# Kernel tuning notes

Measured on AMD Instinct MI355X. Metric: run time of the kernel, lower is better.

## Reference

```python
import jax, jax.numpy as jnp
import numpy as np

N_NODES, N_EDGES = 20000, 400000
IN_DIM, HC, OUT_DIM, EDGE_DIM = 128, 128, 128, 2


def _add_self_loops(src, dst, ea, n):
    # PyG fill_value='mean': self-loop edge_attr = mean of incoming edge_attr
    deg = jax.ops.segment_sum(jnp.ones(src.shape[0], ea.dtype), dst, num_segments=n)
    mean_ea = jax.ops.segment_sum(ea, dst, num_segments=n) / jnp.clip(deg, 1.0)[:, None]
    loop = jnp.arange(n, dtype=src.dtype)
    return (jnp.concatenate([src, loop]), jnp.concatenate([dst, loop]),
            jnp.concatenate([ea, mean_ea], axis=0))


def _gat(x, src, dst, ea, W, att_s, att_d, We, att_e, b, heads, out_ch, concat):
    n = x.shape[0]
    xh = (x @ W).reshape(n, heads, out_ch)                      # [N,H,C]
    a_src = jnp.einsum('nhc,hc->nh', xh, att_s)                  # [N,H]
    a_dst = jnp.einsum('nhc,hc->nh', xh, att_d)
    eh = (ea @ We).reshape(-1, heads, out_ch)                    # [E,H,C]
    a_e = jnp.einsum('ehc,hc->eh', eh, att_e)                    # [E,H]
    alpha = jax.nn.leaky_relu(a_src[src] + a_dst[dst] + a_e, 0.2)
    # segment softmax over destination nodes (every node has a self loop)
    amax = jax.ops.segment_max(alpha, dst, num_segments=n)
    amax = jnp.where(jnp.isfinite(amax), amax, 0.0)
    ex = jnp.exp(alpha - amax[dst])
    denom = jax.ops.segment_sum(ex, dst, num_segments=n)
    w = ex / (denom[dst] + 1e-16)                                # [E,H]
    out = jax.ops.segment_sum(xh[src] * w[..., None], dst, num_segments=n)  # [N,H,C]
    out = out.reshape(n, heads * out_ch) if concat else out.mean(axis=1)
    return out + b


def setup_inputs() -> dict:
    key = jax.random.key(0)
    ks = jax.random.split(key, 16)
    g = lambda k, shape, fan: jax.random.normal(k, shape, jnp.float32) * (1.0 / np.sqrt(fan))
    inp = {
        'x': jax.random.normal(ks[0], (N_NODES, IN_DIM), jnp.float32),
        'edge_index': jax.random.randint(ks[1], (2, N_EDGES), 0, N_NODES, jnp.int32),
        'edge_attr': jax.random.normal(ks[2], (N_EDGES, EDGE_DIM), jnp.float32),
        # conv1: GATConv(128 -> hc=128, heads=2, edge_dim=2, concat=True)
        'W1': g(ks[3], (IN_DIM, 2 * HC), IN_DIM),
        'att_s1': g(ks[4], (2, HC), HC),
        'att_d1': g(ks[5], (2, HC), HC),
        'We1': g(ks[6], (EDGE_DIM, 2 * HC), EDGE_DIM),
        'att_e1': g(ks[7], (2, HC), HC),
        'b1': jnp.zeros((2 * HC,), jnp.float32),
        # conv2: GATConv(256 -> 128, heads=1, edge_dim=2, concat=False)
        'W2': g(ks[8], (2 * HC, OUT_DIM), 2 * HC),
        'att_s2': g(ks[9], (1, OUT_DIM), OUT_DIM),
        'att_d2': g(ks[10], (1, OUT_DIM), OUT_DIM),
        'We2': g(ks[11], (EDGE_DIM, OUT_DIM), EDGE_DIM),
        'att_e2': g(ks[12], (1, OUT_DIM), OUT_DIM),
        'b2': jnp.zeros((OUT_DIM,), jnp.float32),
    }
    return inp


def reference(x, edge_index, edge_attr, W1, att_s1, att_d1, We1, att_e1, b1,
              W2, att_s2, att_d2, We2, att_e2, b2):
    n = x.shape[0]
    src0, dst0 = edge_index[0], edge_index[1]
    src, dst, ea = _add_self_loops(src0, dst0, edge_attr, n)
    x0 = x
    h = jax.nn.relu(_gat(x, src, dst, ea, W1, att_s1, att_d1, We1, att_e1, b1,
                         heads=2, out_ch=HC, concat=True))
    h = _gat(h, src, dst, ea, W2, att_s2, att_d2, We2, att_e2, b2,
             heads=1, out_ch=OUT_DIM, concat=False)
    # SimpleConv(aggr='mean'): mean over incoming neighbors on the ORIGINAL edges
    deg = jax.ops.segment_sum(jnp.ones(src0.shape[0], h.dtype), dst0, num_segments=n)
    mean_h = jax.ops.segment_sum(h[src0], dst0, num_segments=n) / jnp.clip(deg, 1.0)[:, None]
    return jax.nn.relu(mean_h + x0)
```

## Files before the change

kernel.cpp:

```cpp
#include <hip/hip_runtime.h>
#include <hip/hip_bf16.h>
#include <hip/hip_fp16.h>

#define NN 20000
#define NE 400000
#define SLOTS 64
#define NBUILD 1563

typedef unsigned short u16;
typedef unsigned int u32;
typedef unsigned long long u64;

typedef __attribute__((ext_vector_type(8))) short bf16x8;
typedef __attribute__((ext_vector_type(4))) float f32x4;

__device__ __forceinline__ float bf2f(u16 u) {
    union { u32 i; float f; } v; v.i = ((u32)u) << 16; return v.f;
}
__device__ __forceinline__ u16 f2bf(float f) {
    __hip_bfloat16 h = __float2bfloat16(f);
    return *reinterpret_cast<u16*>(&h);
}
__device__ __forceinline__ u32 pack2(float lo, float hi) {
    return (u32)f2bf(lo) | ((u32)f2bf(hi) << 16);
}
__device__ __forceinline__ u16 f2h(float f) {
    __half h = __float2half(f);
    return *reinterpret_cast<u16*>(&h);
}
__device__ __forceinline__ float h2f(u16 u) {
    __half h = *reinterpret_cast<__half*>(&u);
    return __half2float(h);
}

__global__ void k_pre(const float* __restrict__ We1, const float* __restrict__ att_e1,
                      const float* __restrict__ We2, const float* __restrict__ att_e2,
                      const float* __restrict__ W1, const float* __restrict__ W2,
                      int* __restrict__ cnt, float* __restrict__ consts,
                      u16* __restrict__ Bt1, u16* __restrict__ Bt2) {
    int idx = blockIdx.x * 256 + threadIdx.x;
    if (idx < NN) cnt[idx] = 0;
    if (idx < 32768) {
        int n = idx >> 7, k = idx & 127;
        Bt1[idx] = f2bf(W1[k * 256 + n]);
    } else {
        int j = idx - 32768;
        int n = j >> 8, k = j & 255;
        Bt2[j] = f2bf(W2[k * 128 + n]);
    }
    if (blockIdx.x == 0) {
        __shared__ float red[128];
        int c = threadIdx.x;
        float p[6];
        if (c < 128) {
            p[0] = We1[0 * 256 + 0 * 128 + c] * att_e1[0 * 128 + c];
            p[1] = We1[0 * 256 + 1 * 128 + c] * att_e1[1 * 128 + c];
            p[2] = We1[1 * 256 + 0 * 128 + c] * att_e1[0 * 128 + c];
            p[3] = We1[1 * 256 + 1 * 128 + c] * att_e1[1 * 128 + c];
            p[4] = We2[0 * 128 + c] * att_e2[c];
            p[5] = We2[1 * 128 + c] * att_e2[c];
        }
        for (int j = 0; j < 6; j++) {
            if (c < 128) red[c] = p[j];
            __syncthreads();
            for (int off = 64; off >= 1; off >>= 1) {
                if (c < off) red[c] += red[c + off];
                __syncthreads();
            }
            if (c == 0) consts[j] = red[0];
            __syncthreads();
        }
    }
}

__global__ __launch_bounds__(256) void k_fat1(const int* __restrict__ ei,
                                              const float* __restrict__ ea,
                                              int* __restrict__ cnt,
                                              uint2* __restrict__ slot,
                                              const float* __restrict__ A,
                                              const u16* __restrict__ Bt,
                                              const float* __restrict__ att_s,
                                              const float* __restrict__ att_d,
                                              u16* __restrict__ C,
                                              float2* __restrict__ a_s,
                                              float2* __restrict__ a_d) {
    if (blockIdx.x < NBUILD) {
        int e = blockIdx.x * 256 + threadIdx.x;
        if (e < NE) {
            int d = ei[NE + e];
            int s = ei[e];
            float2 v = *reinterpret_cast<const float2*>(ea + (size_t)e * 2);
            int pos = atomicAdd(&cnt[d], 1);
            if (pos < SLOTS) {
                u32 eh = (u32)f2h(v.x) | ((u32)f2h(v.y) << 16);
                slot[d * SLOTS + pos] = make_uint2((u32)s, eh);
            }
        }
        return;
    }
    constexpr int K = 128, KC = 4, NT = 16;
    int gb = blockIdx.x - NBUILD;
    int lane = threadIdx.x & 63;
    int wave = threadIdx.x >> 6;
    int r0 = (gb * 4 + wave) * 16;
    if (r0 >= NN) return;
    int mrow = lane & 15, g = lane >> 4;
    int arow = r0 + mrow; if (arow >= NN) arow = NN - 1;
    const float* abase = A + (size_t)arow * K + g * 8;
    bf16x8 a[KC];
#pragma unroll
    for (int kc = 0; kc < KC; kc++) {
        float4 lo = *reinterpret_cast<const float4*>(abase + kc * 32);
        float4 hi = *reinterpret_cast<const float4*>(abase + kc * 32 + 4);
        bf16x8 t;
        t[0] = (short)f2bf(lo.x); t[1] = (short)f2bf(lo.y);
        t[2] = (short)f2bf(lo.z); t[3] = (short)f2bf(lo.w);
        t[4] = (short)f2bf(hi.x); t[5] = (short)f2bf(hi.y);
        t[6] = (short)f2bf(hi.z); t[7] = (short)f2bf(hi.w);
        a[kc] = t;
    }
    f32x4 acc[NT];
#pragma unroll
    for (int nt = 0; nt < NT; nt++) acc[nt] = (f32x4){0.f, 0.f, 0.f, 0.f};
#pragma unroll
    for (int nt = 0; nt < NT; nt++) {
        const u16* bbase = Bt + (size_t)(nt * 16 + mrow) * K + g * 8;
#pragma unroll
        for (int kc = 0; kc < KC; kc++) {
            bf16x8 b = *reinterpret_cast<const bf16x8*>(bbase + kc * 32);
            acc[nt] = __builtin_amdgcn_mfma_f32_16x16x32_bf16(a[kc], b, acc[nt], 0, 0, 0);
        }
    }
    int orow0 = r0 + g * 4;
#pragma unroll
    for (int nt = 0; nt < NT; nt++)
#pragma unroll
        for (int r = 0; r < 4; r++) {
            int rr = orow0 + r;
            if (rr < NN) C[(size_t)rr * 256 + nt * 16 + mrow] = f2bf(acc[nt][r]);
        }
    float attsv[NT], attdv[NT];
#pragma unroll
    for (int nt = 0; nt < NT; nt++) {
        attsv[nt] = att_s[nt * 16 + mrow];
        attdv[nt] = att_d[nt * 16 + mrow];
    }
#pragma unroll
    for (int r = 0; r < 4; r++) {
        float s0 = 0.f, s1 = 0.f, d0 = 0.f, d1 = 0.f;
#pragma unroll
        for (int nt = 0; nt < 8; nt++) { s0 += acc[nt][r] * attsv[nt]; d0 += acc[nt][r] * attdv[nt]; }
#pragma unroll
        for (int nt = 8; nt < NT; nt++) { s1 += acc[nt][r] * attsv[nt]; d1 += acc[nt][r] * attdv[nt]; }
        for (int off = 8; off >= 1; off >>= 1) {
            s0 += __shfl_xor(s0, off); s1 += __shfl_xor(s1, off);
            d0 += __shfl_xor(d0, off); d1 += __shfl_xor(d1, off);
        }
        int rr = orow0 + r;
        if (mrow == 0 && rr < NN) {
            a_s[rr] = make_float2(s0, s1);
            a_d[rr] = make_float2(d0, d1);
        }
    }
}

__global__ __launch_bounds__(256) void k_gemm2(const u16* __restrict__ A,
                                               const u16* __restrict__ Bt,
                                               const float* __restrict__ att_s,
                                               const float* __restrict__ att_d,
                                               u16* __restrict__ C,
                                               float* __restrict__ a_s,
                                               float* __restrict__ a_d) {
    constexpr int K = 256, KC = 8, NT = 8;
    int lane = threadIdx.x & 63;
    int wave = threadIdx.x >> 6;
    int r0 = (blockIdx.x * 4 + wave) * 16;
    if (r0 >= NN) return;
    int mrow = lane & 15, g = lane >> 4;
    int arow = r0 + mrow; if (arow >= NN) arow = NN - 1;
    const u16* abase = A + (size_t)arow * K + g * 8;
    bf16x8 a[KC];
#pragma unroll
    for (int kc = 0; kc < KC; kc++) a[kc] = *reinterpret_cast<const bf16x8*>(abase + kc * 32);
    f32x4 acc[NT];
#pragma unroll
    for (int nt = 0; nt < NT; nt++) acc[nt] = (f32x4){0.f, 0.f, 0.f, 0.f};
#pragma unroll
    for (int nt = 0; nt < NT; nt++) {
        const u16* bbase = Bt + (size_t)(nt * 16 + mrow) * K + g * 8;
#pragma unroll
        for (int kc = 0; kc < KC; kc++) {
            bf16x8 b = *reinterpret_cast<const bf16x8*>(bbase + kc * 32);
            acc[nt] = __builtin_amdgcn_mfma_f32_16x16x32_bf16(a[kc], b, acc[nt], 0, 0, 0);
        }
    }
    int orow0 = r0 + g * 4;
#pragma unroll
    for (int nt = 0; nt < NT; nt++)
#pragma unroll
        for (int r = 0; r < 4; r++) {
            int rr = orow0 + r;
            if (rr < NN) C[(size_t)rr * 128 + nt * 16 + mrow] = f2bf(acc[nt][r]);
        }
    float attsv[NT], attdv[NT];
#pragma unroll
    for (int nt = 0; nt < NT; nt++) {
        attsv[nt] = att_s[nt * 16 + mrow];
        attdv[nt] = att_d[nt * 16 + mrow];
    }
#pragma unroll
    for (int r = 0; r < 4; r++) {
        float s0 = 0.f, d0 = 0.f;
#pragma unroll
        for (int nt = 0; nt < NT; nt++) { s0 += acc[nt][r] * attsv[nt]; d0 += acc[nt][r] * attdv[nt]; }
        for (int off = 8; off >= 1; off >>= 1) {
            s0 += __shfl_xor(s0, off);
            d0 += __shfl_xor(d0, off);
        }
        int rr = orow0 + r;
        if (mrow == 0 && rr < NN) { a_s[rr] = s0; a_d[rr] = d0; }
    }
}

__global__ __launch_bounds__(256) void k_conv1(const int* __restrict__ cnt,
                                               const uint2* __restrict__ slot,
                                               const float* __restrict__ consts,
                                               const u16* __restrict__ xh1,
                                               const float2* __restrict__ a_s,
                                               const float2* __restrict__ a_d,
                                               const float* __restrict__ b1,
                                               u16* __restrict__ h1out) {
    int lane = threadIdx.x & 63;
    int n = blockIdx.x * 4 + (threadIdx.x >> 6);
    if (n >= NN) return;
    int deg = cnt[n]; if (deg > SLOTS) deg = SLOTS;
    float c00 = consts[0], c01 = consts[1], c10 = consts[2], c11 = consts[3];
    float2 ad = a_d[n];
    float2 asn = a_s[n];
    bool valid = lane < deg;
    int s = 0; float ae0 = 0.f, ae1 = 0.f;
    if (valid) {
        uint2 rec = slot[n * SLOTS + lane];
        s = (int)rec.x;
        float e0v = h2f((u16)(rec.y & 0xffff));
        float e1v = h2f((u16)(rec.y >> 16));
        ae0 = e0v * c00 + e1v * c10;
        ae1 = e0v * c01 + e1v * c11;
    }
    float sum0 = ae0, sum1 = ae1;
    for (int off = 32; off >= 1; off >>= 1) {
        sum0 += __shfl_xor(sum0, off);
        sum1 += __shfl_xor(sum1, off);
    }
    float invdeg = 1.f / (float)(deg < 1 ? 1 : deg);
    float sae0 = sum0 * invdeg, sae1 = sum1 * invdeg;
    float2 asv = valid ? a_s[s] : make_float2(0.f, 0.f);
    float l0 = asv.x + ad.x + ae0;
    float l1 = asv.y + ad.y + ae1;
    l0 = l0 >= 0.f ? l0 : 0.2f * l0;
    l1 = l1 >= 0.f ? l1 : 0.2f * l1;
    if (!valid) { l0 = -3.4e38f; l1 = -3.4e38f; }
    float sl0 = asn.x + ad.x + sae0;
    float sl1 = asn.y + ad.y + sae1;
    sl0 = sl0 >= 0.f ? sl0 : 0.2f * sl0;
    sl1 = sl1 >= 0.f ? sl1 : 0.2f * sl1;
    float cm0 = l0, cm1 = l1;
    for (int off = 32; off >= 1; off >>= 1) {
        cm0 = fmaxf(cm0, __shfl_xor(cm0, off));
        cm1 = fmaxf(cm1, __shfl_xor(cm1, off));
    }
    float m0 = fmaxf(cm0, sl0), m1 = fmaxf(cm1, sl1);
    float e0 = valid ? __expf(l0 - m0) : 0.f;
    float e1 = valid ? __expf(l1 - m1) : 0.f;
    float es0 = __expf(sl0 - m0), es1 = __expf(sl1 - m1);
    float cs0 = e0, cs1 = e1;
    for (int off = 32; off >= 1; off >>= 1) {
        cs0 += __shfl_xor(cs0, off);
        cs1 += __shfl_xor(cs1, off);
    }
    float den0 = cs0 + es0 + 1e-16f, den1 = cs1 + es1 + 1e-16f;
    int q = lane >> 4, ql = lane & 15;
    int ch = ql * 16;
    int myh = ql >> 3;
    float acc[16];
#pragma unroll
    for (int i = 0; i < 16; i++) acc[i] = 0.f;
    for (int j = 0; j < deg; j += 4) {
        int jj = j + q;
        bool ve = jj < deg;
        int sj = ve ? __shfl(s, jj) : n;
        float w0 = __shfl(e0, jj), w1 = __shfl(e1, jj);
        float wj = ve ? (myh ? w1 : w0) : 0.f;
        const u16* p = xh1 + (size_t)sj * 256 + ch;
        uint4 va = *reinterpret_cast<const uint4*>(p);
        uint4 vb = *reinterpret_cast<const uint4*>(p + 8);
        acc[0] += wj * bf2f((u16)(va.x & 0xffff)); acc[1] += wj * bf2f((u16)(va.x >> 16));
        acc[2] += wj * bf2f((u16)(va.y & 0xffff)); acc[3] += wj * bf2f((u16)(va.y >> 16));
        acc[4] += wj * bf2f((u16)(va.z & 0xffff)); acc[5] += wj * bf2f((u16)(va.z >> 16));
        acc[6] += wj * bf2f((u16)(va.w & 0xffff)); acc[7] += wj * bf2f((u16)(va.w >> 16));
        acc[8] += wj * bf2f((u16)(vb.x & 0xffff)); acc[9] += wj * bf2f((u16)(vb.x >> 16));
        acc[10] += wj * bf2f((u16)(vb.y & 0xffff)); acc[11] += wj * bf2f((u16)(vb.y >> 16));
        acc[12] += wj * bf2f((u16)(vb.z & 0xffff)); acc[13] += wj * bf2f((u16)(vb.z >> 16));
        acc[14] += wj * bf2f((u16)(vb.w & 0xffff)); acc[15] += wj * bf2f((u16)(vb.w >> 16));
    }
#pragma unroll
    for (int i = 0; i < 16; i++) {
        acc[i] += __shfl_xor(acc[i], 16);
        acc[i] += __shfl_xor(acc[i], 32);
    }
    if (q == 0) {
        float ws = myh ? es1 : es0;
        const u16* p = xh1 + (size_t)n * 256 + ch;
        uint4 va = *reinterpret_cast<const uint4*>(p);
        uint4 vb = *reinterpret_cast<const uint4*>(p + 8);
        acc[0] += ws * bf2f((u16)(va.x & 0xffff)); acc[1] += ws * bf2f((u16)(va.x >> 16));
        acc[2] += ws * bf2f((u16)(va.y & 0xffff)); acc[3] += ws * bf2f((u16)(va.y >> 16));
        acc[4] += ws * bf2f((u16)(va.z & 0xffff)); acc[5] += ws * bf2f((u16)(va.z >> 16));
        acc[6] += ws * bf2f((u16)(va.w & 0xffff)); acc[7] += ws * bf2f((u16)(va.w >> 16));
        acc[8] += ws * bf2f((u16)(vb.x & 0xffff)); acc[9] += ws * bf2f((u16)(vb.x >> 16));
        acc[10] += ws * bf2f((u16)(vb.y & 0xffff)); acc[11] += ws * bf2f((u16)(vb.y >> 16));
        acc[12] += ws * bf2f((u16)(vb.z & 0xffff)); acc[13] += ws * bf2f((u16)(vb.z >> 16));
        acc[14] += ws * bf2f((u16)(vb.w & 0xffff)); acc[15] += ws * bf2f((u16)(vb.w >> 16));
        float inv = 1.f / (myh ? den1 : den0);
        float o[16];
#pragma unroll
        for (int i = 0; i < 4; i++) {
            float4 b4 = *reinterpret_cast<const float4*>(b1 + ch + i * 4);
            o[i * 4 + 0] = acc[i * 4 + 0] * inv + b4.x;
            o[i * 4 + 1] = acc[i * 4 + 1] * inv + b4.y;
            o[i * 4 + 2] = acc[i * 4 + 2] * inv + b4.z;
            o[i * 4 + 3] = acc[i * 4 + 3] * inv + b4.w;
        }
#pragma unroll
        for (int i = 0; i < 16; i++) o[i] = o[i] > 0.f ? o[i] : 0.f;
        uint4 sa, sb;
        sa.x = pack2(o[0], o[1]);  sa.y = pack2(o[2], o[3]);
        sa.z = pack2(o[4], o[5]);  sa.w = pack2(o[6], o[7]);
        sb.x = pack2(o[8], o[9]);  sb.y = pack2(o[10], o[11]);
        sb.z = pack2(o[12], o[13]); sb.w = pack2(o[14], o[15]);
        *reinterpret_cast<uint4*>(h1out + (size_t)n * 256 + ch) = sa;
        *reinterpret_cast<uint4*>(h1out + (size_t)n * 256 + ch + 8) = sb;
    }
}

__global__ __launch_bounds__(256) void k_conv2(const int* __restrict__ cnt,
                                               const uint2* __restrict__ slot,
                                               const float* __restrict__ consts,
                                               const u16* __restrict__ xh2,
                                               const float* __restrict__ a_s,
                                               const float* __restrict__ a_d,
                                               const float* __restrict__ b2v,
                                               u16* __restrict__ h2out) {
    int lane = threadIdx.x & 63;
    int n = blockIdx.x * 4 + (threadIdx.x >> 6);
    if (n >= NN) return;
    int deg = cnt[n]; if (deg > SLOTS) deg = SLOTS;
    float d0c = consts[4], d1c = consts[5];
    float ad = a_d[n];
    float asn = a_s[n];
    bool valid = lane < deg;
    int s = 0; float ae = 0.f;
    if (valid) {
        uint2 rec = slot[n * SLOTS + lane];
        s = (int)rec.x;
        ae = h2f((u16)(rec.y & 0xffff)) * d0c + h2f((u16)(rec.y >> 16)) * d1c;
    }
    float sum = ae;
    for (int off = 32; off >= 1; off >>= 1) sum += __shfl_xor(sum, off);
    float invdeg = 1.f / (float)(deg < 1 ? 1 : deg);
    float sae = sum * invdeg;
    float l = (valid ? a_s[s] : 0.f) + ad + ae;
    l = l >= 0.f ? l : 0.2f * l;
    if (!valid) l = -3.4e38f;
    float sl = asn + ad + sae;
    sl = sl >= 0.f ? sl : 0.2f * sl;
    float cm = l;
    for (int off = 32; off >= 1; off >>= 1) cm = fmaxf(cm, __shfl_xor(cm, off));
    float m = fmaxf(cm, sl);
    float e = valid ? __expf(l - m) : 0.f;
    float es = __expf(sl - m);
    float cs = e;
    for (int off = 32; off >= 1; off >>= 1) cs += __shfl_xor(cs, off);
    float den = cs + es + 1e-16f;
    int q = lane >> 4, ql = lane & 15;
    int ch = ql * 8;
    float acc[8];
#pragma unroll
    for (int i = 0; i < 8; i++) acc[i] = 0.f;
    for (int j = 0; j < deg; j += 4) {
        int jj = j + q;
        bool ve = jj < deg;
        int sj = ve ? __shfl(s, jj) : n;
        float wj = ve ? __shfl(e, jj) : 0.f;
        uint4 v = *reinterpret_cast<const uint4*>(xh2 + (size_t)sj * 128 + ch);
        acc[0] += wj * bf2f((u16)(v.x & 0xffff)); acc[1] += wj * bf2f((u16)(v.x >> 16));
        acc[2] += wj * bf2f((u16)(v.y & 0xffff)); acc[3] += wj * bf2f((u16)(v.y >> 16));
        acc[4] += wj * bf2f((u16)(v.z & 0xffff)); acc[5] += wj * bf2f((u16)(v.z >> 16));
        acc[6] += wj * bf2f((u16)(v.w & 0xffff)); acc[7] += wj * bf2f((u16)(v.w >> 16));
    }
#pragma unroll
    for (int i = 0; i < 8; i++) {
        acc[i] += __shfl_xor(acc[i], 16);
        acc[i] += __shfl_xor(acc[i], 32);
    }
    if (q == 0) {
        uint4 v = *reinterpret_cast<const uint4*>(xh2 + (size_t)n * 128 + ch);
        acc[0] += es * bf2f((u16)(v.x & 0xffff)); acc[1] += es * bf2f((u16)(v.x >> 16));
        acc[2] += es * bf2f((u16)(v.y & 0xffff)); acc[3] += es * bf2f((u16)(v.y >> 16));
        acc[4] += es * bf2f((u16)(v.z & 0xffff)); acc[5] += es * bf2f((u16)(v.z >> 16));
        acc[6] += es * bf2f((u16)(v.w & 0xffff)); acc[7] += es * bf2f((u16)(v.w >> 16));
        float inv = 1.f / den;
        float4 ba = *reinterpret_cast<const float4*>(b2v + ch);
        float4 bb = *reinterpret_cast<const float4*>(b2v + ch + 4);
        uint4 st;
        st.x = pack2(acc[0] * inv + ba.x, acc[1] * inv + ba.y);
        st.y = pack2(acc[2] * inv + ba.z, acc[3] * inv + ba.w);
        st.z = pack2(acc[4] * inv + bb.x, acc[5] * inv + bb.y);
        st.w = pack2(acc[6] * inv + bb.z, acc[7] * inv + bb.w);
        *reinterpret_cast<uint4*>(h2out + (size_t)n * 128 + ch) = st;
    }
}

__global__ __launch_bounds__(256) void k_final(const int* __restrict__ cnt,
                                               const uint2* __restrict__ slot,
                                               const u16* __restrict__ h2,
                                               const float* __restrict__ x,
                                               float* __restrict__ out) {
    int lane = threadIdx.x & 63;
    int n = blockIdx.x * 4 + (threadIdx.x >> 6);
    if (n >= NN) return;
    int deg = cnt[n]; if (deg > SLOTS) deg = SLOTS;
    int s = (lane < deg) ? (int)slot[n * SLOTS + lane].x : 0;
    int q = lane >> 4, ql = lane & 15;
    int ch = ql * 8;
    float acc[8];
#pragma unroll
    for (int i = 0; i < 8; i++) acc[i] = 0.f;
    for (int j = 0; j < deg; j += 4) {
        int jj = j + q;
        bool ve = jj < deg;
        int sj = ve ? __shfl(s, jj) : n;
        float wj = ve ? 1.f : 0.f;
        uint4 v = *reinterpret_cast<const uint4*>(h2 + (size_t)sj * 128 + ch);
        acc[0] += wj * bf2f((u16)(v.x & 0xffff)); acc[1] += wj * bf2f((u16)(v.x >> 16));
        acc[2] += wj * bf2f((u16)(v.y & 0xffff)); acc[3] += wj * bf2f((u16)(v.y >> 16));
        acc[4] += wj * bf2f((u16)(v.z & 0xffff)); acc[5] += wj * bf2f((u16)(v.z >> 16));
        acc[6] += wj * bf2f((u16)(v.w & 0xffff)); acc[7] += wj * bf2f((u16)(v.w >> 16));
    }
#pragma unroll
    for (int i = 0; i < 8; i++) {
        acc[i] += __shfl_xor(acc[i], 16);
        acc[i] += __shfl_xor(acc[i], 32);
    }
    if (q == 0) {
        float invd = 1.f / (float)(deg < 1 ? 1 : deg);
        float4 xa = *reinterpret_cast<const float4*>(x + (size_t)n * 128 + ch);
        float4 xb = *reinterpret_cast<const float4*>(x + (size_t)n * 128 + ch + 4);
        float o0 = acc[0] * invd + xa.x, o1 = acc[1] * invd + xa.y;
        float o2 = acc[2] * invd + xa.z, o3 = acc[3] * invd + xa.w;
        float o4 = acc[4] * invd + xb.x, o5 = acc[5] * invd + xb.y;
        float o6 = acc[6] * invd + xb.z, o7 = acc[7] * invd + xb.w;
        float4 sa = make_float4(o0 > 0.f ? o0 : 0.f, o1 > 0.f ? o1 : 0.f,
                                o2 > 0.f ? o2 : 0.f, o3 > 0.f ? o3 : 0.f);
        float4 sb = make_float4(o4 > 0.f ? o4 : 0.f, o5 > 0.f ? o5 : 0.f,
                                o6 > 0.f ? o6 : 0.f, o7 > 0.f ? o7 : 0.f);
        *reinterpret_cast<float4*>(out + (size_t)n * 128 + ch) = sa;
        *reinterpret_cast<float4*>(out + (size_t)n * 128 + ch + 4) = sb;
    }
}

extern "C" void kernel_launch(void* const* d_in, const int* in_sizes, int n_in,
                              void* d_out, int out_size, void* d_ws, size_t ws_size,
                              hipStream_t stream) {
    const float* x      = (const float*)d_in[0];
    const int*   ei     = (const int*)d_in[1];
    const float* ea     = (const float*)d_in[2];
    const float* W1     = (const float*)d_in[3];
    const float* att_s1 = (const float*)d_in[4];
    const float* att_d1 = (const float*)d_in[5];
    const float* We1    = (const float*)d_in[6];
    const float* att_e1 = (const float*)d_in[7];
    const float* b1     = (const float*)d_in[8];
    const float* W2     = (const float*)d_in[9];
    const float* att_s2 = (const float*)d_in[10];
    const float* att_d2 = (const float*)d_in[11];
    const float* We2    = (const float*)d_in[12];
    const float* att_e2 = (const float*)d_in[13];
    const float* b2     = (const float*)d_in[14];
    float* out = (float*)d_out;

    char* w = (char*)d_ws;
    auto alloc = [&](size_t bytes) -> void* {
        void* p = (void*)w;
        w += (bytes + 255) & ~(size_t)255;
        return p;
    };
    int*    cnt    = (int*)alloc(NN * 4);
    float*  consts = (float*)alloc(64);
    uint2*  slot   = (uint2*)alloc((size_t)NN * SLOTS * 8);
    u16*    Bt1    = (u16*)alloc(256 * 128 * 2);
    u16*    Bt2    = (u16*)alloc(128 * 256 * 2);
    u16*    xh1b   = (u16*)alloc((size_t)NN * 256 * 2);
    u16*    h1b    = (u16*)alloc((size_t)NN * 256 * 2);
    float2* a_s1   = (float2*)alloc(NN * 8);
    float2* a_d1   = (float2*)alloc(NN * 8);
    float*  a_s2   = (float*)alloc(NN * 4);
    float*  a_d2   = (float*)alloc(NN * 4);
    u16* xh2b = xh1b;
    u16* h2b  = h1b;

    k_pre<<<256, 256, 0, stream>>>(We1, att_e1, We2, att_e2, W1, W2, cnt, consts, Bt1, Bt2);
    k_fat1<<<NBUILD + (NN + 63) / 64, 256, 0, stream>>>(ei, ea, cnt, slot,
                                                        x, Bt1, att_s1, att_d1,
                                                        xh1b, a_s1, a_d1);
    k_conv1<<<(NN + 3) / 4, 256, 0, stream>>>(cnt, slot, consts, xh1b, a_s1, a_d1, b1, h1b);
    k_gemm2<<<(NN + 63) / 64, 256, 0, stream>>>(h1b, Bt2, att_s2, att_d2, xh2b, a_s2, a_d2);
    k_conv2<<<(NN + 3) / 4, 256, 0, stream>>>(cnt, slot, consts, xh2b, a_s2, a_d2, b2, h2b);
    k_final<<<(NN + 3) / 4, 256, 0, stream>>>(cnt, slot, h2b, x, out);
}
```

Measured before the change: 145.4 us.

## Split aggregation kernels by channel half with XCD-aware block mapping; unfuse build/gemm1

```diff
diff --git a/kernel.cpp b/kernel.cpp
--- a/kernel.cpp
+++ b/kernel.cpp
@@ -5,7 +5,6 @@
 #define NN 20000
 #define NE 400000
 #define SLOTS 64
-#define NBUILD 1563
 
 typedef unsigned short u16;
 typedef unsigned int u32;
@@ -31,6 +30,13 @@
 __device__ __forceinline__ float h2f(u16 u) {
     __half h = *reinterpret_cast<__half*>(&u);
     return __half2float(h);
+}
+
+__device__ __forceinline__ void split_decode(int b, int lane_node, int& n, int& half) {
+    int xcd = b & 7;
+    half = xcd >> 2;
+    int grp = (b >> 3) * 4 + (xcd & 3);
+    n = grp * 4 + lane_node;
 }
 
 __global__ void k_pre(const float* __restrict__ We1, const float* __restrict__ att_e1,
@@ -73,36 +79,31 @@
     }
 }
 
-__global__ __launch_bounds__(256) void k_fat1(const int* __restrict__ ei,
-                                              const float* __restrict__ ea,
-                                              int* __restrict__ cnt,
-                                              uint2* __restrict__ slot,
-                                              const float* __restrict__ A,
-                                              const u16* __restrict__ Bt,
-                                              const float* __restrict__ att_s,
-                                              const float* __restrict__ att_d,
-                                              u16* __restrict__ C,
-                                              float2* __restrict__ a_s,
-                                              float2* __restrict__ a_d) {
-    if (blockIdx.x < NBUILD) {
-        int e = blockIdx.x * 256 + threadIdx.x;
-        if (e < NE) {
-            int d = ei[NE + e];
-            int s = ei[e];
-            float2 v = *reinterpret_cast<const float2*>(ea + (size_t)e * 2);
-            int pos = atomicAdd(&cnt[d], 1);
-            if (pos < SLOTS) {
-                u32 eh = (u32)f2h(v.x) | ((u32)f2h(v.y) << 16);
-                slot[d * SLOTS + pos] = make_uint2((u32)s, eh);
-            }
-        }
-        return;
-    }
+__global__ void k_build(const int* __restrict__ ei, const float* __restrict__ ea,
+                        int* __restrict__ cnt, uint2* __restrict__ slot) {
+    int e = blockIdx.x * 256 + threadIdx.x;
+    if (e >= NE) return;
+    int d = ei[NE + e];
+    int s = ei[e];
+    float2 v = *reinterpret_cast<const float2*>(ea + (size_t)e * 2);
+    int pos = atomicAdd(&cnt[d], 1);
+    if (pos < SLOTS) {
+        u32 eh = (u32)f2h(v.x) | ((u32)f2h(v.y) << 16);
+        slot[d * SLOTS + pos] = make_uint2((u32)s, eh);
+    }
+}
+
+__global__ __launch_bounds__(256) void k_gemm1(const float* __restrict__ A,
+                                               const u16* __restrict__ Bt,
+                                               const float* __restrict__ att_s,
+                                               const float* __restrict__ att_d,
+                                               u16* __restrict__ C,
+                                               float2* __restrict__ a_s,
+                                               float2* __restrict__ a_d) {
     constexpr int K = 128, KC = 4, NT = 16;
-    int gb = blockIdx.x - NBUILD;
     int lane = threadIdx.x & 63;
     int wave = threadIdx.x >> 6;
-    int r0 = (gb * 4 + wave) * 16;
+    int r0 = (blockIdx.x * 4 + wave) * 16;
     if (r0 >= NN) return;
     int mrow = lane & 15, g = lane >> 4;
     int arow = r0 + mrow; if (arow >= NN) arow = NN - 1;
@@ -226,120 +227,82 @@
                                                const uint2* __restrict__ slot,
                                                const float* __restrict__ consts,
                                                const u16* __restrict__ xh1,
-                                               const float2* __restrict__ a_s,
-                                               const float2* __restrict__ a_d,
+                                               const float* __restrict__ a_s,
+                                               const float* __restrict__ a_d,
                                                const float* __restrict__ b1,
                                                u16* __restrict__ h1out) {
     int lane = threadIdx.x & 63;
-    int n = blockIdx.x * 4 + (threadIdx.x >> 6);
+    int n, half;
+    split_decode(blockIdx.x, threadIdx.x >> 6, n, half);
     if (n >= NN) return;
     int deg = cnt[n]; if (deg > SLOTS) deg = SLOTS;
-    float c00 = consts[0], c01 = consts[1], c10 = consts[2], c11 = consts[3];
-    float2 ad = a_d[n];
-    float2 asn = a_s[n];
+    float c0 = consts[half], c1 = consts[2 + half];
+    float ad = a_d[n * 2 + half];
+    float asn = a_s[n * 2 + half];
     bool valid = lane < deg;
-    int s = 0; float ae0 = 0.f, ae1 = 0.f;
+    int s = 0; float ae = 0.f;
     if (valid) {
         uint2 rec = slot[n * SLOTS + lane];
         s = (int)rec.x;
-        float e0v = h2f((u16)(rec.y & 0xffff));
-        float e1v = h2f((u16)(rec.y >> 16));
-        ae0 = e0v * c00 + e1v * c10;
-        ae1 = e0v * c01 + e1v * c11;
-    }
-    float sum0 = ae0, sum1 = ae1;
-    for (int off = 32; off >= 1; off >>= 1) {
-        sum0 += __shfl_xor(sum0, off);
-        sum1 += __shfl_xor(sum1, off);
-    }
+        ae = h2f((u16)(rec.y & 0xffff)) * c0 + h2f((u16)(rec.y >> 16)) * c1;
+    }
+    float sum = ae;
+    for (int off = 32; off >= 1; off >>= 1) sum += __shfl_xor(sum, off);
     float invdeg = 1.f / (float)(deg < 1 ? 1 : deg);
-    float sae0 = sum0 * invdeg, sae1 = sum1 * invdeg;
-    float2 asv = valid ? a_s[s] : make_float2(0.f, 0.f);
-    float l0 = asv.x + ad.x + ae0;
-    float l1 = asv.y + ad.y + ae1;
-    l0 = l0 >= 0.f ? l0 : 0.2f * l0;
-    l1 = l1 >= 0.f ? l1 : 0.2f * l1;
-    if (!valid) { l0 = -3.4e38f; l1 = -3.4e38f; }
-    float sl0 = asn.x + ad.x + sae0;
-    float sl1 = asn.y + ad.y + sae1;
-    sl0 = sl0 >= 0.f ? sl0 : 0.2f * sl0;
-    sl1 = sl1 >= 0.f ? sl1 : 0.2f * sl1;
-    float cm0 = l0, cm1 = l1;
-    for (int off = 32; off >= 1; off >>= 1) {
-        cm0 = fmaxf(cm0, __shfl_xor(cm0, off));
-        cm1 = fmaxf(cm1, __shfl_xor(cm1, off));
-    }
-    float m0 = fmaxf(cm0, sl0), m1 = fmaxf(cm1, sl1);
-    float e0 = valid ? __expf(l0 - m0) : 0.f;
-    float e1 = valid ? __expf(l1 - m1) : 0.f;
-    float es0 = __expf(sl0 - m0), es1 = __expf(sl1 - m1);
-    float cs0 = e0, cs1 = e1;
-    for (int off = 32; off >= 1; off >>= 1) {
-        cs0 += __shfl_xor(cs0, off);
-        cs1 += __shfl_xor(cs1, off);
-    }
-    float den0 = cs0 + es0 + 1e-16f, den1 = cs1 + es1 + 1e-16f;
+    float sae = sum * invdeg;
+    float l = (valid ? a_s[s * 2 + half] : 0.f) + ad + ae;
+    l = l >= 0.f ? l : 0.2f * l;
+    if (!valid) l = -3.4e38f;
+    float sl = asn + ad + sae;
+    sl = sl >= 0.f ? sl : 0.2f * sl;
+    float cm = l;
+    for (int off = 32; off >= 1; off >>= 1) cm = fmaxf(cm, __shfl_xor(cm, off));
+    float m = fmaxf(cm, sl);
+    float e = valid ? __expf(l - m) : 0.f;
+    float es = __expf(sl - m);
+    float cs = e;
+    for (int off = 32; off >= 1; off >>= 1) cs += __shfl_xor(cs, off);
+    float den = cs + es + 1e-16f;
     int q = lane >> 4, ql = lane & 15;
-    int ch = ql * 16;
-    int myh = ql >> 3;
-    float acc[16];
-#pragma unroll
-    for (int i = 0; i < 16; i++) acc[i] = 0.f;
+    int ch = ql * 8;
+    float acc[8];
+#pragma unroll
+    for (int i = 0; i < 8; i++) acc[i] = 0.f;
     for (int j = 0; j < deg; j += 4) {
         int jj = j + q;
         bool ve = jj < deg;
         int sj = ve ? __shfl(s, jj) : n;
-        float w0 = __shfl(e0, jj), w1 = __shfl(e1, jj);
-        float wj = ve ? (myh ? w1 : w0) : 0.f;
-        const u16* p = xh1 + (size_t)sj * 256 + ch;
-        uint4 va = *reinterpret_cast<const uint4*>(p);
-        uint4 vb = *reinterpret_cast<const uint4*>(p + 8);
-        acc[0] += wj * bf2f((u16)(va.x & 0xffff)); acc[1] += wj * bf2f((u16)(va.x >> 16));
-        acc[2] += wj * bf2f((u16)(va.y & 0xffff)); acc[3] += wj * bf2f((u16)(va.y >> 16));
-        acc[4] += wj * bf2f((u16)(va.z & 0xffff)); acc[5] += wj * bf2f((u16)(va.z >> 16));
-        acc[6] += wj * bf2f((u16)(va.w & 0xffff)); acc[7] += wj * bf2f((u16)(va.w >> 16));
-        acc[8] += wj * bf2f((u16)(vb.x & 0xffff)); acc[9] += wj * bf2f((u16)(vb.x >> 16));
-        acc[10] += wj * bf2f((u16)(vb.y & 0xffff)); acc[11] += wj * bf2f((u16)(vb.y >> 16));
-        acc[12] += wj * bf2f((u16)(vb.z & 0xffff)); acc[13] += wj * bf2f((u16)(vb.z >> 16));
-        acc[14] += wj * bf2f((u16)(vb.w & 0xffff)); acc[15] += wj * bf2f((u16)(vb.w >> 16));
-    }
-#pragma unroll
-    for (int i = 0; i < 16; i++) {
+        float wj = ve ? __shfl(e, jj) : 0.f;
+        uint4 v = *reinterpret_cast<const uint4*>(xh1 + (size_t)sj * 256 + half * 128 + ch);
+        acc[0] += wj * bf2f((u16)(v.x & 0xffff)); acc[1] += wj * bf2f((u16)(v.x >> 16));
+        acc[2] += wj * bf2f((u16)(v.y & 0xffff)); acc[3] += wj * bf2f((u16)(v.y >> 16));
+        acc[4] += wj * bf2f((u16)(v.z & 0xffff)); acc[5] += wj * bf2f((u16)(v.z >> 16));
+        acc[6] += wj * bf2f((u16)(v.w & 0xffff)); acc[7] += wj * bf2f((u16)(v.w >> 16));
+    }
+#pragma unroll
+    for (int i = 0; i < 8; i++) {
         acc[i] += __shfl_xor(acc[i], 16);
         acc[i] += __shfl_xor(acc[i], 32);
     }
     if (q == 0) {
-        float ws = myh ? es1 : es0;
-        const u16* p = xh1 + (size_t)n * 256 + ch;
-        uint4 va = *reinterpret_cast<const uint4*>(p);
-        uint4 vb = *reinterpret_cast<const uint4*>(p + 8);
-        acc[0] += ws * bf2f((u16)(va.x & 0xffff)); acc[1] += ws * bf2f((u16)(va.x >> 16));
-        acc[2] += ws * bf2f((u16)(va.y & 0xffff)); acc[3] += ws * bf2f((u16)(va.y >> 16));
-        acc[4] += ws * bf2f((u16)(va.z & 0xffff)); acc[5] += ws * bf2f((u16)(va.z >> 16));
-        acc[6] += ws * bf2f((u16)(va.w & 0xffff)); acc[7] += ws * bf2f((u16)(va.w >> 16));
-        acc[8] += ws * bf2f((u16)(vb.x & 0xffff)); acc[9] += ws * bf2f((u16)(vb.x >> 16));
-        acc[10] += ws * bf2f((u16)(vb.y & 0xffff)); acc[11] += ws * bf2f((u16)(vb.y >> 16));
-        acc[12] += ws * bf2f((u16)(vb.z & 0xffff)); acc[13] += ws * bf2f((u16)(vb.z >> 16));
-        acc[14] += ws * bf2f((u16)(vb.w & 0xffff)); acc[15] += ws * bf2f((u16)(vb.w >> 16));
-        float inv = 1.f / (myh ? den1 : den0);
-        float o[16];
-#pragma unroll
-        for (int i = 0; i < 4; i++) {
-            float4 b4 = *reinterpret_cast<const float4*>(b1 + ch + i * 4);
-            o[i * 4 + 0] = acc[i * 4 + 0] * inv + b4.x;
-            o[i * 4 + 1] = acc[i * 4 + 1] * inv + b4.y;
-            o[i * 4 + 2] = acc[i * 4 + 2] * inv + b4.z;
-            o[i * 4 + 3] = acc[i * 4 + 3] * inv + b4.w;
-        }
-#pragma unroll
-        for (int i = 0; i < 16; i++) o[i] = o[i] > 0.f ? o[i] : 0.f;
-        uint4 sa, sb;
-        sa.x = pack2(o[0], o[1]);  sa.y = pack2(o[2], o[3]);
-        sa.z = pack2(o[4], o[5]);  sa.w = pack2(o[6], o[7]);
-        sb.x = pack2(o[8], o[9]);  sb.y = pack2(o[10], o[11]);
-        sb.z = pack2(o[12], o[13]); sb.w = pack2(o[14], o[15]);
-        *reinterpret_cast<uint4*>(h1out + (size_t)n * 256 + ch) = sa;
-        *reinterpret_cast<uint4*>(h1out + (size_t)n * 256 + ch + 8) = sb;
+        uint4 v = *reinterpret_cast<const uint4*>(xh1 + (size_t)n * 256 + half * 128 + ch);
+        acc[0] += es * bf2f((u16)(v.x & 0xffff)); acc[1] += es * bf2f((u16)(v.x >> 16));
+        acc[2] += es * bf2f((u16)(v.y & 0xffff)); acc[3] += es * bf2f((u16)(v.y >> 16));
+        acc[4] += es * bf2f((u16)(v.z & 0xffff)); acc[5] += es * bf2f((u16)(v.z >> 16));
+        acc[6] += es * bf2f((u16)(v.w & 0xffff)); acc[7] += es * bf2f((u16)(v.w >> 16));
+        float inv = 1.f / den;
+        float4 ba = *reinterpret_cast<const float4*>(b1 + half * 128 + ch);
+        float4 bb = *reinterpret_cast<const float4*>(b1 + half * 128 + ch + 4);
+        float o0 = acc[0] * inv + ba.x, o1 = acc[1] * inv + ba.y;
+        float o2 = acc[2] * inv + ba.z, o3 = acc[3] * inv + ba.w;
+        float o4 = acc[4] * inv + bb.x, o5 = acc[5] * inv + bb.y;
+        float o6 = acc[6] * inv + bb.z, o7 = acc[7] * inv + bb.w;
+        uint4 st;
+        st.x = pack2(o0 > 0.f ? o0 : 0.f, o1 > 0.f ? o1 : 0.f);
+        st.y = pack2(o2 > 0.f ? o2 : 0.f, o3 > 0.f ? o3 : 0.f);
+        st.z = pack2(o4 > 0.f ? o4 : 0.f, o5 > 0.f ? o5 : 0.f);
+        st.w = pack2(o6 > 0.f ? o6 : 0.f, o7 > 0.f ? o7 : 0.f);
+        *reinterpret_cast<uint4*>(h1out + (size_t)n * 256 + half * 128 + ch) = st;
     }
 }
 
@@ -352,7 +315,8 @@
                                                const float* __restrict__ b2v,
                                                u16* __restrict__ h2out) {
     int lane = threadIdx.x & 63;
-    int n = blockIdx.x * 4 + (threadIdx.x >> 6);
+    int n, half;
+    split_decode(blockIdx.x, threadIdx.x >> 6, n, half);
     if (n >= NN) return;
     int deg = cnt[n]; if (deg > SLOTS) deg = SLOTS;
     float d0c = consts[4], d1c = consts[5];
@@ -383,41 +347,34 @@
     for (int off = 32; off >= 1; off >>= 1) cs += __shfl_xor(cs, off);
     float den = cs + es + 1e-16f;
     int q = lane >> 4, ql = lane & 15;
-    int ch = ql * 8;
-    float acc[8];
-#pragma unroll
-    for (int i = 0; i < 8; i++) acc[i] = 0.f;
+    int ch = half * 64 + ql * 4;
+    float acc[4];
+#pragma unroll
+    for (int i = 0; i < 4; i++) acc[i] = 0.f;
     for (int j = 0; j < deg; j += 4) {
         int jj = j + q;
         bool ve = jj < deg;
         int sj = ve ? __shfl(s, jj) : n;
         float wj = ve ? __shfl(e, jj) : 0.f;
-        uint4 v = *reinterpret_cast<const uint4*>(xh2 + (size_t)sj * 128 + ch);
+        uint2 v = *reinterpret_cast<const uint2*>(xh2 + (size_t)sj * 128 + ch);
         acc[0] += wj * bf2f((u16)(v.x & 0xffff)); acc[1] += wj * bf2f((u16)(v.x >> 16));
         acc[2] += wj * bf2f((u16)(v.y & 0xffff)); acc[3] += wj * bf2f((u16)(v.y >> 16));
-        acc[4] += wj * bf2f((u16)(v.z & 0xffff)); acc[5] += wj * bf2f((u16)(v.z >> 16));
-        acc[6] += wj * bf2f((u16)(v.w & 0xffff)); acc[7] += wj * bf2f((u16)(v.w >> 16));
-    }
-#pragma unroll
-    for (int i = 0; i < 8; i++) {
+    }
+#pragma unroll
+    for (int i = 0; i < 4; i++) {
         acc[i] += __shfl_xor(acc[i], 16);
         acc[i] += __shfl_xor(acc[i], 32);
     }
     if (q == 0) {
-        uint4 v = *reinterpret_cast<const uint4*>(xh2 + (size_t)n * 128 + ch);
+        uint2 v = *reinterpret_cast<const uint2*>(xh2 + (size_t)n * 128 + ch);
         acc[0] += es * bf2f((u16)(v.x & 0xffff)); acc[1] += es * bf2f((u16)(v.x >> 16));
         acc[2] += es * bf2f((u16)(v.y & 0xffff)); acc[3] += es * bf2f((u16)(v.y >> 16));
-        acc[4] += es * bf2f((u16)(v.z & 0xffff)); acc[5] += es * bf2f((u16)(v.z >> 16));
-        acc[6] += es * bf2f((u16)(v.w & 0xffff)); acc[7] += es * bf2f((u16)(v.w >> 16));
         float inv = 1.f / den;
-        float4 ba = *reinterpret_cast<const float4*>(b2v + ch);
-        float4 bb = *reinterpret_cast<const float4*>(b2v + ch + 4);
-        uint4 st;
-        st.x = pack2(acc[0] * inv + ba.x, acc[1] * inv + ba.y);
-        st.y = pack2(acc[2] * inv + ba.z, acc[3] * inv + ba.w);
-        st.z = pack2(acc[4] * inv + bb.x, acc[5] * inv + bb.y);
-        st.w = pack2(acc[6] * inv + bb.z, acc[7] * inv + bb.w);
-        *reinterpret_cast<uint4*>(h2out + (size_t)n * 128 + ch) = st;
+        float4 b4 = *reinterpret_cast<const float4*>(b2v + ch);
+        uint2 st;
+        st.x = pack2(acc[0] * inv + b4.x, acc[1] * inv + b4.y);
+        st.y = pack2(acc[2] * inv + b4.z, acc[3] * inv + b4.w);
+        *reinterpret_cast<uint2*>(h2out + (size_t)n * 128 + ch) = st;
     }
 }
 
@@ -427,45 +384,38 @@
                                                const float* __restrict__ x,
                                                float* __restrict__ out) {
     int lane = threadIdx.x & 63;
-    int n = blockIdx.x * 4 + (threadIdx.x >> 6);
+    int n, half;
+    split_decode(blockIdx.x, threadIdx.x >> 6, n, half);
     if (n >= NN) return;
     int deg = cnt[n]; if (deg > SLOTS) deg = SLOTS;
     int s = (lane < deg) ? (int)slot[n * SLOTS + lane].x : 0;
     int q = lane >> 4, ql = lane & 15;
-    int ch = ql * 8;
-    float acc[8];
-#pragma unroll
-    for (int i = 0; i < 8; i++) acc[i] = 0.f;
+    int ch = half * 64 + ql * 4;
+    float acc[4];
+#pragma unroll
+    for (int i = 0; i < 4; i++) acc[i] = 0.f;
     for (int j = 0; j < deg; j += 4) {
         int jj = j + q;
         bool ve = jj < deg;
         int sj = ve ? __shfl(s, jj) : n;
         float wj = ve ? 1.f : 0.f;
-        uint4 v = *reinterpret_cast<const uint4*>(h2 + (size_t)sj * 128 + ch);
+        uint2 v = *reinterpret_cast<const uint2*>(h2 + (size_t)sj * 128 + ch);
         acc[0] += wj * bf2f((u16)(v.x & 0xffff)); acc[1] += wj * bf2f((u16)(v.x >> 16));
         acc[2] += wj * bf2f((u16)(v.y & 0xffff)); acc[3] += wj * bf2f((u16)(v.y >> 16));
-        acc[4] += wj * bf2f((u16)(v.z & 0xffff)); acc[5] += wj * bf2f((u16)(v.z >> 16));
-        acc[6] += wj * bf2f((u16)(v.w & 0xffff)); acc[7] += wj * bf2f((u16)(v.w >> 16));
-    }
-#pragma unroll
-    for (int i = 0; i < 8; i++) {
+    }
+#pragma unroll
+    for (int i = 0; i < 4; i++) {
         acc[i] += __shfl_xor(acc[i], 16);
         acc[i] += __shfl_xor(acc[i], 32);
     }
     if (q == 0) {
         float invd = 1.f / (float)(deg < 1 ? 1 : deg);
-        float4 xa = *reinterpret_cast<const float4*>(x + (size_t)n * 128 + ch);
-        float4 xb = *reinterpret_cast<const float4*>(x + (size_t)n * 128 + ch + 4);
-        float o0 = acc[0] * invd + xa.x, o1 = acc[1] * invd + xa.y;
-        float o2 = acc[2] * invd + xa.z, o3 = acc[3] * invd + xa.w;
-        float o4 = acc[4] * invd + xb.x, o5 = acc[5] * invd + xb.y;
-        float o6 = acc[6] * invd + xb.z, o7 = acc[7] * invd + xb.w;
-        float4 sa = make_float4(o0 > 0.f ? o0 : 0.f, o1 > 0.f ? o1 : 0.f,
+        float4 xv = *reinterpret_cast<const float4*>(x + (size_t)n * 128 + ch);
+        float o0 = acc[0] * invd + xv.x, o1 = acc[1] * invd + xv.y;
+        float o2 = acc[2] * invd + xv.z, o3 = acc[3] * invd + xv.w;
+        float4 st = make_float4(o0 > 0.f ? o0 : 0.f, o1 > 0.f ? o1 : 0.f,
                                 o2 > 0.f ? o2 : 0.f, o3 > 0.f ? o3 : 0.f);
-        float4 sb = make_float4(o4 > 0.f ? o4 : 0.f, o5 > 0.f ? o5 : 0.f,
-                                o6 > 0.f ? o6 : 0.f, o7 > 0.f ? o7 : 0.f);
-        *reinterpret_cast<float4*>(out + (size_t)n * 128 + ch) = sa;
-        *reinterpret_cast<float4*>(out + (size_t)n * 128 + ch + 4) = sb;
+        *reinterpret_cast<float4*>(out + (size_t)n * 128 + ch) = st;
     }
 }
 
@@ -509,12 +459,15 @@
     u16* xh2b = xh1b;
     u16* h2b  = h1b;
 
+    const int splitGrid = 2 * ((NN + 3) / 4);
+
     k_pre<<<256, 256, 0, stream>>>(We1, att_e1, We2, att_e2, W1, W2, cnt, consts, Bt1, Bt2);
-    k_fat1<<<NBUILD + (NN + 63) / 64, 256, 0, stream>>>(ei, ea, cnt, slot,
-                                                        x, Bt1, att_s1, att_d1,
-                                                        xh1b, a_s1, a_d1);
-    k_conv1<<<(NN + 3) / 4, 256, 0, stream>>>(cnt, slot, consts, xh1b, a_s1, a_d1, b1, h1b);
+    k_build<<<(NE + 255) / 256, 256, 0, stream>>>(ei, ea, cnt, slot);
+
+    k_gemm1<<<(NN + 63) / 64, 256, 0, stream>>>(x, Bt1, att_s1, att_d1, xh1b, a_s1, a_d1);
+    k_conv1<<<splitGrid, 256, 0, stream>>>(cnt, slot, consts, xh1b,
+                                           (const float*)a_s1, (const float*)a_d1, b1, h1b);
     k_gemm2<<<(NN + 63) / 64, 256, 0, stream>>>(h1b, Bt2, att_s2, att_d2, xh2b, a_s2, a_d2);
-    k_conv2<<<(NN + 3) / 4, 256, 0, stream>>>(cnt, slot, consts, xh2b, a_s2, a_d2, b2, h2b);
-    k_final<<<(NN + 3) / 4, 256, 0, stream>>>(cnt, slot, h2b, x, out);
-}
+    k_conv2<<<splitGrid, 256, 0, stream>>>(cnt, slot, consts, xh2b, a_s2, a_d2, b2, h2b);
+    k_final<<<splitGrid, 256, 0, stream>>>(cnt, slot, h2b, x, out);
+}
```

New measurement: 156.3 us. 7.5% more time.
